# Optimization experiments

Measured on AMD Instinct MI355X. Metric: run time of the kernel, lower is better.

The kernel has to match this reference:

```python
import math
import jax, jax.numpy as jnp
import numpy as np

N_HEAD = 16
BLOCK_SIZE = 2048


def setup_inputs() -> dict:
    key = jax.random.key(0)
    ks = jax.random.split(key, 6)
    B, L, D = 2, 2048, 1024
    hs = D // N_HEAD
    s = 0.02
    return {
        "x": jax.random.normal(ks[0], (B, L, D), dtype=jnp.float32),
        "Wqkv": jax.random.normal(ks[1], (D, 3 * D), dtype=jnp.float32) * s,
        "bqkv": jax.random.normal(ks[2], (3 * D,), dtype=jnp.float32) * s,
        "Wproj": jax.random.normal(ks[3], (D, D), dtype=jnp.float32) * s,
        "bproj": jax.random.normal(ks[4], (D,), dtype=jnp.float32) * s,
        "Er": jax.random.normal(ks[5], (BLOCK_SIZE, hs), dtype=jnp.float32),
    }


def _skew(QEr):
    # QEr: [B, H, L, L] -> pad one zero column on the left, reshape, drop first row
    B, H, R, C = QEr.shape
    padded = jnp.pad(QEr, ((0, 0), (0, 0), (0, 0), (1, 0)))  # [B,H,R,C+1]
    reshaped = padded.reshape(B, H, C + 1, R)
    return reshaped[:, :, 1:, :]  # [B,H,R,C]


def reference(x, Wqkv, bqkv, Wproj, bproj, Er):
    B, L, D = x.shape
    H = N_HEAD
    hs = D // H
    qkv = x @ Wqkv + bqkv  # [B,L,3D]
    q, k, v = jnp.split(qkv, 3, axis=-1)
    q = q.reshape(B, L, H, hs).transpose(0, 2, 1, 3)  # [B,H,L,hs]
    k = k.reshape(B, L, H, hs).transpose(0, 2, 1, 3)
    v = v.reshape(B, L, H, hs).transpose(0, 2, 1, 3)

    Er_used = Er[BLOCK_SIZE - L:, :]           # [L, hs]
    QEr = jnp.einsum('bhld,md->bhlm', q, Er_used)  # q @ Er^T -> [B,H,L,L]
    Srel = _skew(QEr)

    scale = 1.0 / math.sqrt(hs)
    att = (jnp.einsum('bhld,bhmd->bhlm', q, k) + Srel) * scale
    causal = jnp.tril(jnp.ones((L, L), dtype=bool))
    att = jnp.where(causal[None, None], att, -jnp.inf)
    att = jax.nn.softmax(att, axis=-1)
    y = jnp.einsum('bhlm,bhmd->bhld', att, v)  # [B,H,L,hs]
    y = y.transpose(0, 2, 1, 3).reshape(B, L, D)
    return y @ Wproj + bproj
```

## Files before the change

### kernel.cpp

```cpp
#include <hip/hip_runtime.h>
#include <hip/hip_bf16.h>

#define LSEQ 2048
#define NH 16
#define HS 64
#define DIM 1024

typedef __attribute__((ext_vector_type(8))) short short8;
typedef __attribute__((ext_vector_type(4))) float f32x4;

typedef const __attribute__((address_space(1))) void g_void_t;
typedef __attribute__((address_space(3))) void s_void_t;

#define QSCALE 0.18033688011112042f

static __device__ __forceinline__ short f2bf(float f) {
  __hip_bfloat16 h = __float2bfloat16(f);
  return __builtin_bit_cast(short, h);
}

static __device__ __forceinline__ float fexp2(float x) {
#if __has_builtin(__builtin_amdgcn_exp2f)
  return __builtin_amdgcn_exp2f(x);
#else
  float r; asm("v_exp_f32 %0, %1" : "=v"(r) : "v"(x)); return r;
#endif
}

template<int CTRL>
static __device__ __forceinline__ float dpp_mov(float x) {
  return __builtin_bit_cast(float,
      __builtin_amdgcn_update_dpp(0, __builtin_bit_cast(int, x), CTRL, 0xF, 0xF, true));
}
static __device__ __forceinline__ float redmax16(float x) {
  x = fmaxf(x, dpp_mov<0xB1>(x));
  x = fmaxf(x, dpp_mov<0x4E>(x));
  x = fmaxf(x, dpp_mov<0x141>(x));
  x = fmaxf(x, dpp_mov<0x140>(x));
  return x;
}
static __device__ __forceinline__ float redsum16(float x) {
  x += dpp_mov<0xB1>(x);
  x += dpp_mov<0x4E>(x);
  x += dpp_mov<0x141>(x);
  x += dpp_mov<0x140>(x);
  return x;
}


__global__ void prep_kernel(const float* __restrict__ x, const float* __restrict__ Er,
                            const float* __restrict__ Wqkv, const float* __restrict__ Wproj,
                            short* __restrict__ xb, short* __restrict__ Erb,
                            short* __restrict__ WqkvT, short* __restrict__ WprojT) {
  __shared__ float tile[64][65];
  int bid = blockIdx.x;
  if (bid < 4224) {
    const float* in; short* out; int i0;
    if (bid < 4096) { in = x;  out = xb;  i0 = bid * 256; }
    else            { in = Er; out = Erb; i0 = (bid - 4096) * 256; }
    int i = i0 + threadIdx.x;
    float4 v = reinterpret_cast<const float4*>(in)[i];
    short4 o;
    o.x = f2bf(v.x); o.y = f2bf(v.y); o.z = f2bf(v.z); o.w = f2bf(v.w);
    reinterpret_cast<short4*>(out)[i] = o;
    return;
  }
  int id = bid - 4224;
  const float* W; short* Wt; int N, tx, ty;
  if (id < 768) { W = Wqkv;  Wt = WqkvT;  N = 3072; tx = id % 48; ty = id / 48; }
  else { id -= 768; W = Wproj; Wt = WprojT; N = 1024; tx = id % 16; ty = id / 16; }
  const int K = 1024;
  int k0 = ty * 64, n0 = tx * 64;
  int t = threadIdx.x;
  int r4 = t >> 6, cc = t & 63;
  for (int i = 0; i < 16; ++i) {
    int row = i * 4 + r4;
    tile[row][cc] = W[(size_t)(k0 + row) * N + (n0 + cc)];
  }
  __syncthreads();
  for (int i = 0; i < 16; ++i) {
    int row = i * 4 + r4;
    Wt[(size_t)(n0 + row) * K + (k0 + cc)] = f2bf(tile[cc][row]);
  }
}


template<int MODE>
__global__ __launch_bounds__(256, 2) void gemm_bt_kernel(
    const short* __restrict__ A, const short* __restrict__ Bt,
    const float* __restrict__ bias, int M, int N, int K,
    short* __restrict__ oq, short* __restrict__ ok, short* __restrict__ ov,
    float* __restrict__ of)
{
  __shared__ short Al[128 * 32];
  __shared__ short Bl[128 * 32];
  const int m0 = blockIdx.y * 128, n0 = blockIdx.x * 128;
  const int t = threadIdx.x;
  const int lane = t & 63, wave = t >> 6;
  const int wr = wave >> 1, wc = wave & 1;
  const int g = lane >> 4, c = lane & 15;
  f32x4 acc[4][4] = {};

  for (int k0 = 0; k0 < K; k0 += 32) {
    __syncthreads();
    for (int i = 0; i < 2; ++i) {
      int ch = i * 256 + t;
      int row = ch >> 2, c8 = ch & 3;
      __builtin_amdgcn_global_load_lds(
          (g_void_t*)(A + (size_t)(m0 + row) * K + k0 + c8 * 8),
          (s_void_t*)(Al + (i * 256 + wave * 64) * 8), 16, 0, 0);
      __builtin_amdgcn_global_load_lds(
          (g_void_t*)(Bt + (size_t)(n0 + row) * K + k0 + c8 * 8),
          (s_void_t*)(Bl + (i * 256 + wave * 64) * 8), 16, 0, 0);
    }
    __syncthreads();
    short8 af[4], bf[4];
#pragma unroll
    for (int mi = 0; mi < 4; ++mi) {
      int row = wr * 64 + mi * 16 + c;
      af[mi] = *reinterpret_cast<const short8*>(Al + row * 32 + g * 8);
    }
#pragma unroll
    for (int ni = 0; ni < 4; ++ni) {
      int row = wc * 64 + ni * 16 + c;
      bf[ni] = *reinterpret_cast<const short8*>(Bl + row * 32 + g * 8);
    }
#pragma unroll
    for (int mi = 0; mi < 4; ++mi)
#pragma unroll
      for (int ni = 0; ni < 4; ++ni)
        acc[mi][ni] = __builtin_amdgcn_mfma_f32_16x16x32_bf16(af[mi], bf[ni], acc[mi][ni], 0, 0, 0);
  }

#pragma unroll
  for (int mi = 0; mi < 4; ++mi)
#pragma unroll
    for (int ni = 0; ni < 4; ++ni) {
      int n = n0 + wc * 64 + ni * 16 + c;
      float bv = bias[n];
#pragma unroll
      for (int r = 0; r < 4; ++r) {
        int m = m0 + wr * 64 + mi * 16 + g * 4 + r;
        float val = acc[mi][ni][r] + bv;
        if (MODE == 0) {
          int which = n >> 10;
          int hh2 = (n >> 6) & 15;
          int d = n & 63;
          int b = m >> 11, ll = m & 2047;
          if (which == 0) {
            oq[(((size_t)b * NH + hh2) * LSEQ + ll) * HS + d] = f2bf(val * QSCALE);
          } else if (which == 1) {
            ok[(((size_t)b * NH + hh2) * LSEQ + ll) * HS + d] = f2bf(val);
          } else {
            ov[(((size_t)b * NH + hh2) * HS + d) * LSEQ + ll] = f2bf(val);
          }
        } else {
          of[(size_t)m * N + n] = val;
        }
      }
    }
}


__global__ __launch_bounds__(256, 2) void attn_kernel(
    const short* __restrict__ Qb, const short* __restrict__ Kb,
    const short* __restrict__ VTb, const short* __restrict__ Erb,
    short* __restrict__ Y)
{
  const int bid = blockIdx.x;
  const int pair = bid >> 5;
  const int bh = bid & 31;
  const int bb = bh >> 4, hh = bh & 15;
  const int t = threadIdx.x;
  const int lane = t & 63, wave = t >> 6;
  const int g = lane >> 4, c = lane & 15;
  const int r8 = lane >> 3;
  const int c16b = (lane & 7) * 16;

  __shared__ short Ql[64 * 64];
  __shared__ short Kl[2][64 * 64];
  __shared__ short Vl[2][64 * 64];
  __shared__ short El[4][64 * 64];
  __shared__ short Pl[4][16 * 64];

  auto process = [&](int qt) {
    const int l0 = qt * 64;
    const int base = 31 - qt;

    const short* Qg = Qb + ((size_t)bh * LSEQ + l0) * HS;
    for (int i = 0; i < 2; ++i) {
      int ch = i * 256 + t;
      int row = ch >> 3, c8 = ch & 7;
      uint4 v = *reinterpret_cast<const uint4*>(Qg + row * HS + c8 * 8);
      int byte = row * 128 + ((c8 * 16) ^ ((row & 7) << 4));
      *reinterpret_cast<uint4*>(reinterpret_cast<char*>(Ql) + byte) = v;
    }
    __syncthreads();

    short8 qf[2];
#pragma unroll
    for (int kk = 0; kk < 2; ++kk) {
      int row = wave * 16 + c;
      int byte = row * 128 + ((kk * 32 + g * 8) * 2 ^ ((row & 7) << 4));
      qf[kk] = *reinterpret_cast<const short8*>(reinterpret_cast<char*>(Ql) + byte);
    }

    f32x4 acc_o[4] = {};
    float mrun[4], lrun[4];
#pragma unroll
    for (int r = 0; r < 4; ++r) { mrun[r] = -1e30f; lrun[r] = 0.0f; }

    auto stage_KV = [&](int step, int sel) {
      const char* Kg = (const char*)(Kb + ((size_t)bh * LSEQ + step * 64) * HS);
#pragma unroll
      for (int j = 0; j < 2; ++j) {
        int row = wave * 16 + j * 8 + r8;
        __builtin_amdgcn_global_load_lds(
            (g_void_t*)(Kg + row * 128 + (c16b ^ ((row & 7) << 4))),
            (s_void_t*)(&Kl[sel][(wave * 16 + j * 8) * 64]), 16, 0, 0);
      }
#pragma unroll
      for (int j = 0; j < 2; ++j) {
        int row = wave * 16 + j * 8 + r8;
        const char* Vg = (const char*)(VTb + ((size_t)bh * HS + row) * LSEQ + step * 64);
        __builtin_amdgcn_global_load_lds(
            (g_void_t*)(Vg + (c16b ^ ((row & 7) << 4))),
            (s_void_t*)(&Vl[sel][(wave * 16 + j * 8) * 64]), 16, 0, 0);
      }
    };
    auto stage_E = [&](int chunk) {
      int slot = chunk & 3;
#pragma unroll
      for (int j = 0; j < 2; ++j) {
        int row = wave * 16 + j * 8 + r8;
        int e = chunk * 64 + row;
        if (e > LSEQ - 1) e = LSEQ - 1;
        __builtin_amdgcn_global_load_lds(
            (g_void_t*)((const char*)Erb + (size_t)e * 128 + (c16b ^ ((row & 7) << 4))),
            (s_void_t*)(&El[slot][(wave * 16 + j * 8) * 64]), 16, 0, 0);
      }
    };

    stage_KV(0, 0);
    stage_E(base);
    stage_E(base + 1);

    for (int s = 0; s <= qt; ++s) {
      const int sel = s & 1;
      const bool diag = (s == qt);

      if (s < qt) {
        stage_KV(s + 1, sel ^ 1);
        stage_E(base + s + 2);
        asm volatile("s_waitcnt vmcnt(6)" ::: "memory");
      } else {
        asm volatile("s_waitcnt vmcnt(0)" ::: "memory");
      }
      __builtin_amdgcn_s_barrier();
      __builtin_amdgcn_sched_barrier(0);

      __builtin_amdgcn_s_setprio(1);
      f32x4 ga[5];
#pragma unroll
      for (int s5 = 0; s5 < 5; ++s5) {
        int rb = ((3 - wave) + s5) * 16 + c;
        int phys = (((base + s + (rb >> 6)) & 3) << 6) | (rb & 63);
        ga[s5] = (f32x4){0.0f, 0.0f, 0.0f, 0.0f};
#pragma unroll
        for (int kk = 0; kk < 2; ++kk) {
          int byte = phys * 128 + (((kk * 32 + g * 8) * 2) ^ ((rb & 7) << 4));
          short8 ef = *reinterpret_cast<const short8*>((char*)El + byte);
          ga[s5] = __builtin_amdgcn_mfma_f32_16x16x32_bf16(qf[kk], ef, ga[s5], 0, 0, 0);
        }
      }

      f32x4 sa[4];
#pragma unroll
      for (int ns = 0; ns < 4; ++ns) {
        sa[ns] = (f32x4){0.0f, 0.0f, 0.0f, 0.0f};
#pragma unroll
        for (int kk = 0; kk < 2; ++kk) {
          int row = ns * 16 + c;
          int byte = row * 128 + (((kk * 32 + g * 8) * 2) ^ ((row & 7) << 4));
          short8 kf = *reinterpret_cast<const short8*>((char*)Kl[sel] + byte);
          sa[ns] = __builtin_amdgcn_mfma_f32_16x16x32_bf16(qf[kk], kf, sa[ns], 0, 0, 0);
        }
      }
      __builtin_amdgcn_s_setprio(0);

      float sv[4][4];
#pragma unroll
      for (int r = 0; r < 4; ++r) {
        int i4 = g * 4 + r;
        int u0 = c + 15 - i4;
        int srcl = (g << 4) | (u0 & 15);
        float bp[5];
#pragma unroll
        for (int s5 = 0; s5 < 5; ++s5) bp[s5] = __shfl(ga[s5][r], srcl, 64);
        bool lo = (u0 < 16);
#pragma unroll
        for (int ns = 0; ns < 4; ++ns) {
          float srel = lo ? bp[ns] : bp[ns + 1];
          float xx = sa[ns][r] + srel;
          if (diag && (ns * 16 + c > wave * 16 + i4)) xx = -1e30f;
          sv[ns][r] = xx;
        }
      }

      float mx[4];
      bool need = false;
#pragma unroll
      for (int r = 0; r < 4; ++r) {
        float m = fmaxf(fmaxf(sv[0][r], sv[1][r]), fmaxf(sv[2][r], sv[3][r]));
        mx[r] = redmax16(m);
        need = need || (mx[r] > mrun[r] + 4.0f);
      }
      if (__ballot(need)) {
#pragma unroll
        for (int r = 0; r < 4; ++r) {
          float mnew = fmaxf(mrun[r], mx[r]);
          float al = fexp2(mrun[r] - mnew);
          mrun[r] = mnew;
          lrun[r] *= al;
#pragma unroll
          for (int ns = 0; ns < 4; ++ns) acc_o[ns][r] *= al;
        }
      }
#pragma unroll
      for (int ns = 0; ns < 4; ++ns)
#pragma unroll
        for (int r = 0; r < 4; ++r)
          sv[ns][r] = fexp2(sv[ns][r] - mrun[r]);
#pragma unroll
      for (int r = 0; r < 4; ++r) {
        float s2 = (sv[0][r] + sv[1][r]) + (sv[2][r] + sv[3][r]);
        lrun[r] += redsum16(s2);
      }

      short* Pw = Pl[wave];
#pragma unroll
      for (int ns = 0; ns < 4; ++ns)
#pragma unroll
        for (int r = 0; r < 4; ++r) {
          int row = g * 4 + r;
          int byte = row * 128 + (((ns * 16 + c) * 2) ^ ((row & 7) << 4));
          *reinterpret_cast<short*>(reinterpret_cast<char*>(Pw) + byte) = f2bf(sv[ns][r]);
        }

      __builtin_amdgcn_s_setprio(1);
#pragma unroll
      for (int kk = 0; kk < 2; ++kk) {
        int kbyte = (kk * 32 + g * 8) * 2;
        int byteP = c * 128 + (kbyte ^ ((c & 7) << 4));
        short8 pf = *reinterpret_cast<const short8*>(reinterpret_cast<char*>(Pw) + byteP);
#pragma unroll
        for (int ns = 0; ns < 4; ++ns) {
          int rowV = ns * 16 + c;
          int byteV = rowV * 128 + (kbyte ^ ((rowV & 7) << 4));
          short8 vf = *reinterpret_cast<const short8*>((char*)Vl[sel] + byteV);
          acc_o[ns] = __builtin_amdgcn_mfma_f32_16x16x32_bf16(pf, vf, acc_o[ns], 0, 0, 0);
        }
      }
      __builtin_amdgcn_s_setprio(0);

      __builtin_amdgcn_sched_barrier(0);
      __builtin_amdgcn_s_barrier();
    }

#pragma unroll
    for (int ns = 0; ns < 4; ++ns)
#pragma unroll
      for (int r = 0; r < 4; ++r) {
        int row = g * 4 + r;
        int lg = l0 + wave * 16 + row;
        int d = ns * 16 + c;
        Y[((size_t)bb * LSEQ + lg) * DIM + hh * HS + d] = f2bf(acc_o[ns][r] / lrun[r]);
      }
  };

  process(31 - pair);
  process(pair);
}


extern "C" void kernel_launch(void* const* d_in, const int* in_sizes, int n_in,
                              void* d_out, int out_size, void* d_ws, size_t ws_size,
                              hipStream_t stream)
{
  const float* x     = (const float*)d_in[0];
  const float* Wqkv  = (const float*)d_in[1];
  const float* bqkv  = (const float*)d_in[2];
  const float* Wproj = (const float*)d_in[3];
  const float* bproj = (const float*)d_in[4];
  const float* Er    = (const float*)d_in[5];

  char* ws = (char*)d_ws;
  short* xb     = (short*)(ws + 0);
  short* WqkvT  = (short*)(ws + 8388608);
  short* WprojT = (short*)(ws + 14680064);
  short* Erb    = (short*)(ws + 16777216);
  short* qB     = (short*)(ws + 17039360);
  short* kB     = (short*)(ws + 25427968);
  short* vTB    = (short*)(ws + 33816576);
  short* yB     = (short*)(ws + 42205184);

  prep_kernel<<<dim3(5248), 256, 0, stream>>>(x, Er, Wqkv, Wproj, xb, Erb, WqkvT, WprojT);

  gemm_bt_kernel<0><<<dim3(3072 / 128, 4096 / 128), 256, 0, stream>>>(
      xb, WqkvT, bqkv, 4096, 3072, 1024, qB, kB, vTB, nullptr);

  attn_kernel<<<dim3(512), 256, 0, stream>>>(qB, kB, vTB, Erb, yB);

  gemm_bt_kernel<1><<<dim3(1024 / 128, 4096 / 128), 256, 0, stream>>>(
      yB, WprojT, bproj, 4096, 1024, 1024, nullptr, nullptr, nullptr, (float*)d_out);
}
```

Measured before the change: 147.7 us.

## Enlarge attention query tile to 128 rows with 8 waves sharing K/V/Er staging

```diff
diff --git a/kernel.cpp b/kernel.cpp
--- a/kernel.cpp
+++ b/kernel.cpp
@@ -162,7 +162,7 @@
 }
 
 
-__global__ __launch_bounds__(256, 2) void attn_kernel(
+__global__ __launch_bounds__(512, 1) void attn_kernel(
     const short* __restrict__ Qb, const short* __restrict__ Kb,
     const short* __restrict__ VTb, const short* __restrict__ Erb,
     short* __restrict__ Y)
@@ -177,191 +177,189 @@
   const int r8 = lane >> 3;
   const int c16b = (lane & 7) * 16;
 
-  __shared__ short Ql[64 * 64];
+  __shared__ short Ql[128 * 64];
   __shared__ short Kl[2][64 * 64];
   __shared__ short Vl[2][64 * 64];
   __shared__ short El[4][64 * 64];
-  __shared__ short Pl[4][16 * 64];
+  __shared__ short Pl[8][16 * 64];
 
   auto process = [&](int qt) {
-    const int l0 = qt * 64;
-    const int base = 31 - qt;
-
-    const short* Qg = Qb + ((size_t)bh * LSEQ + l0) * HS;
-    for (int i = 0; i < 2; ++i) {
-      int ch = i * 256 + t;
-      int row = ch >> 3, c8 = ch & 7;
-      uint4 v = *reinterpret_cast<const uint4*>(Qg + row * HS + c8 * 8);
-      int byte = row * 128 + ((c8 * 16) ^ ((row & 7) << 4));
-      *reinterpret_cast<uint4*>(reinterpret_cast<char*>(Ql) + byte) = v;
-    }
-    __syncthreads();
-
-    short8 qf[2];
-#pragma unroll
-    for (int kk = 0; kk < 2; ++kk) {
-      int row = wave * 16 + c;
-      int byte = row * 128 + ((kk * 32 + g * 8) * 2 ^ ((row & 7) << 4));
-      qf[kk] = *reinterpret_cast<const short8*>(reinterpret_cast<char*>(Ql) + byte);
-    }
-
-    f32x4 acc_o[4] = {};
-    float mrun[4], lrun[4];
-#pragma unroll
-    for (int r = 0; r < 4; ++r) { mrun[r] = -1e30f; lrun[r] = 0.0f; }
+    const int l0 = qt * 128;
+    const int base = 30 - 2 * qt;
+    const int nsteps = 2 * qt + 2;
 
     auto stage_KV = [&](int step, int sel) {
+      int row = wave * 8 + r8;
       const char* Kg = (const char*)(Kb + ((size_t)bh * LSEQ + step * 64) * HS);
-#pragma unroll
-      for (int j = 0; j < 2; ++j) {
-        int row = wave * 16 + j * 8 + r8;
-        __builtin_amdgcn_global_load_lds(
-            (g_void_t*)(Kg + row * 128 + (c16b ^ ((row & 7) << 4))),
-            (s_void_t*)(&Kl[sel][(wave * 16 + j * 8) * 64]), 16, 0, 0);
-      }
-#pragma unroll
-      for (int j = 0; j < 2; ++j) {
-        int row = wave * 16 + j * 8 + r8;
-        const char* Vg = (const char*)(VTb + ((size_t)bh * HS + row) * LSEQ + step * 64);
-        __builtin_amdgcn_global_load_lds(
-            (g_void_t*)(Vg + (c16b ^ ((row & 7) << 4))),
-            (s_void_t*)(&Vl[sel][(wave * 16 + j * 8) * 64]), 16, 0, 0);
-      }
+      __builtin_amdgcn_global_load_lds(
+          (g_void_t*)(Kg + row * 128 + (c16b ^ ((row & 7) << 4))),
+          (s_void_t*)(&Kl[sel][(wave * 8) * 64]), 16, 0, 0);
+      const char* Vg = (const char*)(VTb + ((size_t)bh * HS + row) * LSEQ + step * 64);
+      __builtin_amdgcn_global_load_lds(
+          (g_void_t*)(Vg + (c16b ^ ((row & 7) << 4))),
+          (s_void_t*)(&Vl[sel][(wave * 8) * 64]), 16, 0, 0);
     };
     auto stage_E = [&](int chunk) {
       int slot = chunk & 3;
-#pragma unroll
-      for (int j = 0; j < 2; ++j) {
-        int row = wave * 16 + j * 8 + r8;
-        int e = chunk * 64 + row;
-        if (e > LSEQ - 1) e = LSEQ - 1;
-        __builtin_amdgcn_global_load_lds(
-            (g_void_t*)((const char*)Erb + (size_t)e * 128 + (c16b ^ ((row & 7) << 4))),
-            (s_void_t*)(&El[slot][(wave * 16 + j * 8) * 64]), 16, 0, 0);
-      }
+      int row = wave * 8 + r8;
+      int e = chunk * 64 + row;
+      if (e > LSEQ - 1) e = LSEQ - 1;
+      __builtin_amdgcn_global_load_lds(
+          (g_void_t*)((const char*)Erb + (size_t)e * 128 + (c16b ^ ((row & 7) << 4))),
+          (s_void_t*)(&El[slot][(wave * 8) * 64]), 16, 0, 0);
     };
 
+    const char* Qg = (const char*)(Qb + ((size_t)bh * LSEQ + l0) * HS);
+#pragma unroll
+    for (int i = 0; i < 2; ++i) {
+      int row = i * 64 + wave * 8 + r8;
+      __builtin_amdgcn_global_load_lds(
+          (g_void_t*)(Qg + row * 128 + (c16b ^ ((row & 7) << 4))),
+          (s_void_t*)(&Ql[(i * 64 + wave * 8) * 64]), 16, 0, 0);
+    }
     stage_KV(0, 0);
-    stage_E(base);
-    stage_E(base + 1);
-
-    for (int s = 0; s <= qt; ++s) {
+    stage_E(base); stage_E(base + 1); stage_E(base + 2);
+
+    asm volatile("s_waitcnt vmcnt(5)" ::: "memory");
+    __builtin_amdgcn_s_barrier();
+    __builtin_amdgcn_sched_barrier(0);
+
+    short8 qf[2];
+#pragma unroll
+    for (int kk = 0; kk < 2; ++kk) {
+      int row = wave * 16 + c;
+      int byte = row * 128 + (((kk * 32 + g * 8) * 2) ^ ((row & 7) << 4));
+      qf[kk] = *reinterpret_cast<const short8*>((char*)Ql + byte);
+    }
+
+    f32x4 acc_o[4] = {};
+    float mrun[4], lrun[4];
+#pragma unroll
+    for (int r = 0; r < 4; ++r) { mrun[r] = -1e30f; lrun[r] = 0.0f; }
+
+    for (int s = 0; s < nsteps; ++s) {
       const int sel = s & 1;
-      const bool diag = (s == qt);
-
-      if (s < qt) {
+      const int cb = base + s;
+
+      if (s + 1 < nsteps) {
         stage_KV(s + 1, sel ^ 1);
-        stage_E(base + s + 2);
-        asm volatile("s_waitcnt vmcnt(6)" ::: "memory");
+        stage_E(cb + 3);
+        asm volatile("s_waitcnt vmcnt(3)" ::: "memory");
       } else {
         asm volatile("s_waitcnt vmcnt(0)" ::: "memory");
       }
       __builtin_amdgcn_s_barrier();
       __builtin_amdgcn_sched_barrier(0);
 
-      __builtin_amdgcn_s_setprio(1);
-      f32x4 ga[5];
-#pragma unroll
-      for (int s5 = 0; s5 < 5; ++s5) {
-        int rb = ((3 - wave) + s5) * 16 + c;
-        int phys = (((base + s + (rb >> 6)) & 3) << 6) | (rb & 63);
-        ga[s5] = (f32x4){0.0f, 0.0f, 0.0f, 0.0f};
+      const bool deadwave = (s == nsteps - 1) && (wave < 4);
+      if (!deadwave) {
+        const bool maskstep = (s >= 2 * qt);
+
+        __builtin_amdgcn_s_setprio(1);
+        f32x4 ga[5];
+#pragma unroll
+        for (int s5 = 0; s5 < 5; ++s5) {
+          int rb = ((7 - wave) + s5) * 16 + c;
+          int phys = (((cb + (rb >> 6)) & 3) << 6) | (rb & 63);
+          ga[s5] = (f32x4){0.0f, 0.0f, 0.0f, 0.0f};
+#pragma unroll
+          for (int kk = 0; kk < 2; ++kk) {
+            int byte = phys * 128 + (((kk * 32 + g * 8) * 2) ^ ((rb & 7) << 4));
+            short8 ef = *reinterpret_cast<const short8*>((char*)El + byte);
+            ga[s5] = __builtin_amdgcn_mfma_f32_16x16x32_bf16(qf[kk], ef, ga[s5], 0, 0, 0);
+          }
+        }
+
+        f32x4 sa[4];
+#pragma unroll
+        for (int ns = 0; ns < 4; ++ns) {
+          sa[ns] = (f32x4){0.0f, 0.0f, 0.0f, 0.0f};
+#pragma unroll
+          for (int kk = 0; kk < 2; ++kk) {
+            int row = ns * 16 + c;
+            int byte = row * 128 + (((kk * 32 + g * 8) * 2) ^ ((row & 7) << 4));
+            short8 kf = *reinterpret_cast<const short8*>((char*)Kl[sel] + byte);
+            sa[ns] = __builtin_amdgcn_mfma_f32_16x16x32_bf16(qf[kk], kf, sa[ns], 0, 0, 0);
+          }
+        }
+        __builtin_amdgcn_s_setprio(0);
+
+        float sv[4][4];
+#pragma unroll
+        for (int r = 0; r < 4; ++r) {
+          int i4 = g * 4 + r;
+          int u0 = c + 15 - i4;
+          int srcl = (g << 4) | (u0 & 15);
+          float bp[5];
+#pragma unroll
+          for (int s5 = 0; s5 < 5; ++s5) bp[s5] = __shfl(ga[s5][r], srcl, 64);
+          bool lo = (u0 < 16);
+          int thr = (l0 - 64 * s) + wave * 16 + i4;
+#pragma unroll
+          for (int ns = 0; ns < 4; ++ns) {
+            float srel = lo ? bp[ns] : bp[ns + 1];
+            float xx = sa[ns][r] + srel;
+            if (maskstep && (ns * 16 + c > thr)) xx = -1e30f;
+            sv[ns][r] = xx;
+          }
+        }
+
+        float mx[4];
+        bool need = false;
+#pragma unroll
+        for (int r = 0; r < 4; ++r) {
+          float m = fmaxf(fmaxf(sv[0][r], sv[1][r]), fmaxf(sv[2][r], sv[3][r]));
+          mx[r] = redmax16(m);
+          need = need || (mx[r] > mrun[r] + 4.0f);
+        }
+        if (__ballot(need)) {
+#pragma unroll
+          for (int r = 0; r < 4; ++r) {
+            float mnew = fmaxf(mrun[r], mx[r]);
+            float al = fexp2(mrun[r] - mnew);
+            mrun[r] = mnew;
+            lrun[r] *= al;
+#pragma unroll
+            for (int ns = 0; ns < 4; ++ns) acc_o[ns][r] *= al;
+          }
+        }
+#pragma unroll
+        for (int ns = 0; ns < 4; ++ns)
+#pragma unroll
+          for (int r = 0; r < 4; ++r)
+            sv[ns][r] = fexp2(sv[ns][r] - mrun[r]);
+#pragma unroll
+        for (int r = 0; r < 4; ++r) {
+          float s2 = (sv[0][r] + sv[1][r]) + (sv[2][r] + sv[3][r]);
+          lrun[r] += redsum16(s2);
+        }
+
+        short* Pw = Pl[wave];
+#pragma unroll
+        for (int ns = 0; ns < 4; ++ns)
+#pragma unroll
+          for (int r = 0; r < 4; ++r) {
+            int row = g * 4 + r;
+            int byte = row * 128 + (((ns * 16 + c) * 2) ^ ((row & 7) << 4));
+            *reinterpret_cast<short*>(reinterpret_cast<char*>(Pw) + byte) = f2bf(sv[ns][r]);
+          }
+
+        __builtin_amdgcn_s_setprio(1);
 #pragma unroll
         for (int kk = 0; kk < 2; ++kk) {
-          int byte = phys * 128 + (((kk * 32 + g * 8) * 2) ^ ((rb & 7) << 4));
-          short8 ef = *reinterpret_cast<const short8*>((char*)El + byte);
-          ga[s5] = __builtin_amdgcn_mfma_f32_16x16x32_bf16(qf[kk], ef, ga[s5], 0, 0, 0);
-        }
+          int kbyte = (kk * 32 + g * 8) * 2;
+          int byteP = c * 128 + (kbyte ^ ((c & 7) << 4));
+          short8 pf = *reinterpret_cast<const short8*>(reinterpret_cast<char*>(Pw) + byteP);
+#pragma unroll
+          for (int ns = 0; ns < 4; ++ns) {
+            int rowV = ns * 16 + c;
+            int byteV = rowV * 128 + (kbyte ^ ((rowV & 7) << 4));
+            short8 vf = *reinterpret_cast<const short8*>((char*)Vl[sel] + byteV);
+            acc_o[ns] = __builtin_amdgcn_mfma_f32_16x16x32_bf16(pf, vf, acc_o[ns], 0, 0, 0);
+          }
+        }
+        __builtin_amdgcn_s_setprio(0);
       }
-
-      f32x4 sa[4];
-#pragma unroll
-      for (int ns = 0; ns < 4; ++ns) {
-        sa[ns] = (f32x4){0.0f, 0.0f, 0.0f, 0.0f};
-#pragma unroll
-        for (int kk = 0; kk < 2; ++kk) {
-          int row = ns * 16 + c;
-          int byte = row * 128 + (((kk * 32 + g * 8) * 2) ^ ((row & 7) << 4));
-          short8 kf = *reinterpret_cast<const short8*>((char*)Kl[sel] + byte);
-          sa[ns] = __builtin_amdgcn_mfma_f32_16x16x32_bf16(qf[kk], kf, sa[ns], 0, 0, 0);
-        }
-      }
-      __builtin_amdgcn_s_setprio(0);
-
-      float sv[4][4];
-#pragma unroll
-      for (int r = 0; r < 4; ++r) {
-        int i4 = g * 4 + r;
-        int u0 = c + 15 - i4;
-        int srcl = (g << 4) | (u0 & 15);
-        float bp[5];
-#pragma unroll
-        for (int s5 = 0; s5 < 5; ++s5) bp[s5] = __shfl(ga[s5][r], srcl, 64);
-        bool lo = (u0 < 16);
-#pragma unroll
-        for (int ns = 0; ns < 4; ++ns) {
-          float srel = lo ? bp[ns] : bp[ns + 1];
-          float xx = sa[ns][r] + srel;
-          if (diag && (ns * 16 + c > wave * 16 + i4)) xx = -1e30f;
-          sv[ns][r] = xx;
-        }
-      }
-
-      float mx[4];
-      bool need = false;
-#pragma unroll
-      for (int r = 0; r < 4; ++r) {
-        float m = fmaxf(fmaxf(sv[0][r], sv[1][r]), fmaxf(sv[2][r], sv[3][r]));
-        mx[r] = redmax16(m);
-        need = need || (mx[r] > mrun[r] + 4.0f);
-      }
-      if (__ballot(need)) {
-#pragma unroll
-        for (int r = 0; r < 4; ++r) {
-          float mnew = fmaxf(mrun[r], mx[r]);
-          float al = fexp2(mrun[r] - mnew);
-          mrun[r] = mnew;
-          lrun[r] *= al;
-#pragma unroll
-          for (int ns = 0; ns < 4; ++ns) acc_o[ns][r] *= al;
-        }
-      }
-#pragma unroll
-      for (int ns = 0; ns < 4; ++ns)
-#pragma unroll
-        for (int r = 0; r < 4; ++r)
-          sv[ns][r] = fexp2(sv[ns][r] - mrun[r]);
-#pragma unroll
-      for (int r = 0; r < 4; ++r) {
-        float s2 = (sv[0][r] + sv[1][r]) + (sv[2][r] + sv[3][r]);
-        lrun[r] += redsum16(s2);
-      }
-
-      short* Pw = Pl[wave];
-#pragma unroll
-      for (int ns = 0; ns < 4; ++ns)
-#pragma unroll
-        for (int r = 0; r < 4; ++r) {
-          int row = g * 4 + r;
-          int byte = row * 128 + (((ns * 16 + c) * 2) ^ ((row & 7) << 4));
-          *reinterpret_cast<short*>(reinterpret_cast<char*>(Pw) + byte) = f2bf(sv[ns][r]);
-        }
-
-      __builtin_amdgcn_s_setprio(1);
-#pragma unroll
-      for (int kk = 0; kk < 2; ++kk) {
-        int kbyte = (kk * 32 + g * 8) * 2;
-        int byteP = c * 128 + (kbyte ^ ((c & 7) << 4));
-        short8 pf = *reinterpret_cast<const short8*>(reinterpret_cast<char*>(Pw) + byteP);
-#pragma unroll
-        for (int ns = 0; ns < 4; ++ns) {
-          int rowV = ns * 16 + c;
-          int byteV = rowV * 128 + (kbyte ^ ((rowV & 7) << 4));
-          short8 vf = *reinterpret_cast<const short8*>((char*)Vl[sel] + byteV);
-          acc_o[ns] = __builtin_amdgcn_mfma_f32_16x16x32_bf16(pf, vf, acc_o[ns], 0, 0, 0);
-        }
-      }
-      __builtin_amdgcn_s_setprio(0);
 
       __builtin_amdgcn_sched_barrier(0);
       __builtin_amdgcn_s_barrier();
@@ -378,7 +376,7 @@
       }
   };
 
-  process(31 - pair);
+  process(15 - pair);
   process(pair);
 }
 
@@ -409,7 +407,7 @@
   gemm_bt_kernel<0><<<dim3(3072 / 128, 4096 / 128), 256, 0, stream>>>(
       xb, WqkvT, bqkv, 4096, 3072, 1024, qB, kB, vTB, nullptr);
 
-  attn_kernel<<<dim3(512), 256, 0, stream>>>(qB, kB, vTB, Erb, yB);
+  attn_kernel<<<dim3(256), 512, 0, stream>>>(qB, kB, vTB, Erb, yB);
 
   gemm_bt_kernel<1><<<dim3(1024 / 128, 4096 / 128), 256, 0, stream>>>(
       yB, WprojT, bproj, 4096, 1024, 1024, nullptr, nullptr, nullptr, (float*)d_out);
```

Measured after the change: 156.0 us. +5.7%, slower.

## Use 128-row query tiles per block with two 16-row subtiles per wave

Applied to the files above, without the earlier changes.

```diff
diff --git a/kernel.cpp b/kernel.cpp
--- a/kernel.cpp
+++ b/kernel.cpp
@@ -168,218 +168,238 @@
     short* __restrict__ Y)
 {
   const int bid = blockIdx.x;
-  const int pair = bid >> 5;
+  const int qt = (bid < 256) ? (15 - (bid >> 5)) : ((bid - 256) >> 5);
   const int bh = bid & 31;
   const int bb = bh >> 4, hh = bh & 15;
   const int t = threadIdx.x;
-  const int lane = t & 63, wave = t >> 6;
+  const int lane = t & 63, w = t >> 6;
   const int g = lane >> 4, c = lane & 15;
   const int r8 = lane >> 3;
   const int c16b = (lane & 7) * 16;
 
-  __shared__ short Ql[64 * 64];
+  const int l0 = qt * 128;
+  const int c00 = 31 - 2 * qt;
+  const int nsteps = 2 * qt + 2;
+
   __shared__ short Kl[2][64 * 64];
   __shared__ short Vl[2][64 * 64];
   __shared__ short El[4][64 * 64];
-  __shared__ short Pl[4][16 * 64];
-
-  auto process = [&](int qt) {
-    const int l0 = qt * 64;
-    const int base = 31 - qt;
-
-    const short* Qg = Qb + ((size_t)bh * LSEQ + l0) * HS;
-    for (int i = 0; i < 2; ++i) {
-      int ch = i * 256 + t;
-      int row = ch >> 3, c8 = ch & 7;
-      uint4 v = *reinterpret_cast<const uint4*>(Qg + row * HS + c8 * 8);
-      int byte = row * 128 + ((c8 * 16) ^ ((row & 7) << 4));
-      *reinterpret_cast<uint4*>(reinterpret_cast<char*>(Ql) + byte) = v;
-    }
-    __syncthreads();
-
-    short8 qf[2];
-#pragma unroll
-    for (int kk = 0; kk < 2; ++kk) {
-      int row = wave * 16 + c;
-      int byte = row * 128 + ((kk * 32 + g * 8) * 2 ^ ((row & 7) << 4));
-      qf[kk] = *reinterpret_cast<const short8*>(reinterpret_cast<char*>(Ql) + byte);
-    }
-
-    f32x4 acc_o[4] = {};
-    float mrun[4], lrun[4];
-#pragma unroll
-    for (int r = 0; r < 4; ++r) { mrun[r] = -1e30f; lrun[r] = 0.0f; }
-
-    auto stage_KV = [&](int step, int sel) {
+  __shared__ short Pl[4][32 * 64];
+
+  short8 qf[2][2];
+#pragma unroll
+  for (int tt = 0; tt < 2; ++tt)
+#pragma unroll
+    for (int kk = 0; kk < 2; ++kk)
+      qf[tt][kk] = *reinterpret_cast<const short8*>(
+          Qb + ((size_t)bh * LSEQ + l0 + w * 32 + tt * 16 + c) * HS + kk * 32 + g * 8);
+
+  auto stage_KV = [&](int step, int sel) {
+    int row = w * 16 + (r8 & 7) + ((lane >> 6) * 8);
+#pragma unroll
+    for (int j = 0; j < 2; ++j) {
+      int rr = w * 16 + j * 8 + r8;
       const char* Kg = (const char*)(Kb + ((size_t)bh * LSEQ + step * 64) * HS);
-#pragma unroll
-      for (int j = 0; j < 2; ++j) {
-        int row = wave * 16 + j * 8 + r8;
-        __builtin_amdgcn_global_load_lds(
-            (g_void_t*)(Kg + row * 128 + (c16b ^ ((row & 7) << 4))),
-            (s_void_t*)(&Kl[sel][(wave * 16 + j * 8) * 64]), 16, 0, 0);
-      }
-#pragma unroll
-      for (int j = 0; j < 2; ++j) {
-        int row = wave * 16 + j * 8 + r8;
-        const char* Vg = (const char*)(VTb + ((size_t)bh * HS + row) * LSEQ + step * 64);
-        __builtin_amdgcn_global_load_lds(
-            (g_void_t*)(Vg + (c16b ^ ((row & 7) << 4))),
-            (s_void_t*)(&Vl[sel][(wave * 16 + j * 8) * 64]), 16, 0, 0);
-      }
-    };
-    auto stage_E = [&](int chunk) {
-      int slot = chunk & 3;
-#pragma unroll
-      for (int j = 0; j < 2; ++j) {
-        int row = wave * 16 + j * 8 + r8;
-        int e = chunk * 64 + row;
-        if (e > LSEQ - 1) e = LSEQ - 1;
-        __builtin_amdgcn_global_load_lds(
-            (g_void_t*)((const char*)Erb + (size_t)e * 128 + (c16b ^ ((row & 7) << 4))),
-            (s_void_t*)(&El[slot][(wave * 16 + j * 8) * 64]), 16, 0, 0);
-      }
-    };
-
-    stage_KV(0, 0);
-    stage_E(base);
-    stage_E(base + 1);
-
-    for (int s = 0; s <= qt; ++s) {
-      const int sel = s & 1;
-      const bool diag = (s == qt);
-
-      if (s < qt) {
-        stage_KV(s + 1, sel ^ 1);
-        stage_E(base + s + 2);
-        asm volatile("s_waitcnt vmcnt(6)" ::: "memory");
-      } else {
-        asm volatile("s_waitcnt vmcnt(0)" ::: "memory");
-      }
-      __builtin_amdgcn_s_barrier();
-      __builtin_amdgcn_sched_barrier(0);
+      __builtin_amdgcn_global_load_lds(
+          (g_void_t*)(Kg + rr * 128 + (c16b ^ ((rr & 7) << 4))),
+          (s_void_t*)(&Kl[sel][(w * 16 + j * 8) * 64]), 16, 0, 0);
+    }
+#pragma unroll
+    for (int j = 0; j < 2; ++j) {
+      int rr = w * 16 + j * 8 + r8;
+      const char* Vg = (const char*)(VTb + ((size_t)bh * HS + rr) * LSEQ + step * 64);
+      __builtin_amdgcn_global_load_lds(
+          (g_void_t*)(Vg + (c16b ^ ((rr & 7) << 4))),
+          (s_void_t*)(&Vl[sel][(w * 16 + j * 8) * 64]), 16, 0, 0);
+    }
+    (void)row;
+  };
+  auto stage_E = [&](int chunk) {
+    int slot = chunk & 3;
+#pragma unroll
+    for (int j = 0; j < 2; ++j) {
+      int rr = w * 16 + j * 8 + r8;
+      int e = chunk * 64 + rr;
+      if (e > LSEQ - 1) e = LSEQ - 1;
+      if (e < 0) e = 0;
+      __builtin_amdgcn_global_load_lds(
+          (g_void_t*)((const char*)Erb + (size_t)e * 128 + (c16b ^ ((rr & 7) << 4))),
+          (s_void_t*)(&El[slot][(w * 16 + j * 8) * 64]), 16, 0, 0);
+    }
+  };
+
+  stage_KV(0, 0);
+  stage_E(c00 - 1); stage_E(c00); stage_E(c00 + 1);
+
+  f32x4 acc_o[2][4] = {};
+  float mrun[2][4], lrun[2][4];
+#pragma unroll
+  for (int tt = 0; tt < 2; ++tt)
+#pragma unroll
+    for (int r = 0; r < 4; ++r) { mrun[tt][r] = -1e30f; lrun[tt][r] = 0.0f; }
+
+  for (int s = 0; s < nsteps; ++s) {
+    const int sel = s & 1;
+    const int c0 = c00 + s;
+
+    if (s + 1 < nsteps) {
+      stage_KV(s + 1, sel ^ 1);
+      stage_E(c0 + 2);
+      asm volatile("s_waitcnt vmcnt(6)" ::: "memory");
+    } else {
+      asm volatile("s_waitcnt vmcnt(0)" ::: "memory");
+    }
+    __builtin_amdgcn_s_barrier();
+    __builtin_amdgcn_sched_barrier(0);
+
+    const bool deadwave = (s == nsteps - 1) && (w < 2);
+    if (!deadwave) {
+      const bool maskstep = (s >= 2 * qt);
 
       __builtin_amdgcn_s_setprio(1);
-      f32x4 ga[5];
-#pragma unroll
-      for (int s5 = 0; s5 < 5; ++s5) {
-        int rb = ((3 - wave) + s5) * 16 + c;
-        int phys = (((base + s + (rb >> 6)) & 3) << 6) | (rb & 63);
-        ga[s5] = (f32x4){0.0f, 0.0f, 0.0f, 0.0f};
+      f32x4 ga[2][5];
+#pragma unroll
+      for (int tt = 0; tt < 2; ++tt)
+#pragma unroll
+        for (int s5 = 0; s5 < 5; ++s5) ga[tt][s5] = (f32x4){0.0f, 0.0f, 0.0f, 0.0f};
+#pragma unroll
+      for (int u = 0; u < 6; ++u) {
+        int rb = ((2 - 2 * w) + u) * 16 + c;
+        int chunk = c0 + (rb >> 6);
+        int phys = ((chunk & 3) << 6) | (rb & 63);
 #pragma unroll
         for (int kk = 0; kk < 2; ++kk) {
           int byte = phys * 128 + (((kk * 32 + g * 8) * 2) ^ ((rb & 7) << 4));
           short8 ef = *reinterpret_cast<const short8*>((char*)El + byte);
-          ga[s5] = __builtin_amdgcn_mfma_f32_16x16x32_bf16(qf[kk], ef, ga[s5], 0, 0, 0);
-        }
-      }
-
-      f32x4 sa[4];
+          if (u >= 1) ga[0][u - 1] = __builtin_amdgcn_mfma_f32_16x16x32_bf16(qf[0][kk], ef, ga[0][u - 1], 0, 0, 0);
+          if (u <= 4) ga[1][u]     = __builtin_amdgcn_mfma_f32_16x16x32_bf16(qf[1][kk], ef, ga[1][u], 0, 0, 0);
+        }
+      }
+
+      f32x4 sa[2][4];
+#pragma unroll
+      for (int tt = 0; tt < 2; ++tt)
+#pragma unroll
+        for (int ns = 0; ns < 4; ++ns) sa[tt][ns] = (f32x4){0.0f, 0.0f, 0.0f, 0.0f};
 #pragma unroll
       for (int ns = 0; ns < 4; ++ns) {
-        sa[ns] = (f32x4){0.0f, 0.0f, 0.0f, 0.0f};
 #pragma unroll
         for (int kk = 0; kk < 2; ++kk) {
           int row = ns * 16 + c;
           int byte = row * 128 + (((kk * 32 + g * 8) * 2) ^ ((row & 7) << 4));
           short8 kf = *reinterpret_cast<const short8*>((char*)Kl[sel] + byte);
-          sa[ns] = __builtin_amdgcn_mfma_f32_16x16x32_bf16(qf[kk], kf, sa[ns], 0, 0, 0);
+          sa[0][ns] = __builtin_amdgcn_mfma_f32_16x16x32_bf16(qf[0][kk], kf, sa[0][ns], 0, 0, 0);
+          sa[1][ns] = __builtin_amdgcn_mfma_f32_16x16x32_bf16(qf[1][kk], kf, sa[1][ns], 0, 0, 0);
         }
       }
       __builtin_amdgcn_s_setprio(0);
 
-      float sv[4][4];
-#pragma unroll
-      for (int r = 0; r < 4; ++r) {
-        int i4 = g * 4 + r;
-        int u0 = c + 15 - i4;
-        int srcl = (g << 4) | (u0 & 15);
-        float bp[5];
-#pragma unroll
-        for (int s5 = 0; s5 < 5; ++s5) bp[s5] = __shfl(ga[s5][r], srcl, 64);
-        bool lo = (u0 < 16);
-#pragma unroll
-        for (int ns = 0; ns < 4; ++ns) {
-          float srel = lo ? bp[ns] : bp[ns + 1];
-          float xx = sa[ns][r] + srel;
-          if (diag && (ns * 16 + c > wave * 16 + i4)) xx = -1e30f;
-          sv[ns][r] = xx;
-        }
-      }
-
-      float mx[4];
+      float sv[2][4][4];
       bool need = false;
-#pragma unroll
-      for (int r = 0; r < 4; ++r) {
-        float m = fmaxf(fmaxf(sv[0][r], sv[1][r]), fmaxf(sv[2][r], sv[3][r]));
-        mx[r] = redmax16(m);
-        need = need || (mx[r] > mrun[r] + 4.0f);
+      float mx[2][4];
+#pragma unroll
+      for (int tt = 0; tt < 2; ++tt) {
+#pragma unroll
+        for (int r = 0; r < 4; ++r) {
+          int i4 = g * 4 + r;
+          int u0 = c + 15 - i4;
+          int srcl = (g << 4) | (u0 & 15);
+          float bp[5];
+#pragma unroll
+          for (int s5 = 0; s5 < 5; ++s5) bp[s5] = __shfl(ga[tt][s5][r], srcl, 64);
+          bool lo = (u0 < 16);
+          int thr = (l0 - 64 * s) + w * 32 + tt * 16 + i4;
+#pragma unroll
+          for (int ns = 0; ns < 4; ++ns) {
+            float srel = lo ? bp[ns] : bp[ns + 1];
+            float xx = sa[tt][ns][r] + srel;
+            if (maskstep && (ns * 16 + c > thr)) xx = -1e30f;
+            sv[tt][ns][r] = xx;
+          }
+        }
+#pragma unroll
+        for (int r = 0; r < 4; ++r) {
+          float m = fmaxf(fmaxf(sv[tt][0][r], sv[tt][1][r]), fmaxf(sv[tt][2][r], sv[tt][3][r]));
+          mx[tt][r] = redmax16(m);
+          need = need || (mx[tt][r] > mrun[tt][r] + 4.0f);
+        }
       }
       if (__ballot(need)) {
 #pragma unroll
+        for (int tt = 0; tt < 2; ++tt)
+#pragma unroll
+          for (int r = 0; r < 4; ++r) {
+            float mnew = fmaxf(mrun[tt][r], mx[tt][r]);
+            float al = fexp2(mrun[tt][r] - mnew);
+            mrun[tt][r] = mnew;
+            lrun[tt][r] *= al;
+#pragma unroll
+            for (int ns = 0; ns < 4; ++ns) acc_o[tt][ns][r] *= al;
+          }
+      }
+#pragma unroll
+      for (int tt = 0; tt < 2; ++tt) {
+#pragma unroll
+        for (int ns = 0; ns < 4; ++ns)
+#pragma unroll
+          for (int r = 0; r < 4; ++r)
+            sv[tt][ns][r] = fexp2(sv[tt][ns][r] - mrun[tt][r]);
+#pragma unroll
         for (int r = 0; r < 4; ++r) {
-          float mnew = fmaxf(mrun[r], mx[r]);
-          float al = fexp2(mrun[r] - mnew);
-          mrun[r] = mnew;
-          lrun[r] *= al;
-#pragma unroll
-          for (int ns = 0; ns < 4; ++ns) acc_o[ns][r] *= al;
-        }
-      }
-#pragma unroll
-      for (int ns = 0; ns < 4; ++ns)
-#pragma unroll
-        for (int r = 0; r < 4; ++r)
-          sv[ns][r] = fexp2(sv[ns][r] - mrun[r]);
-#pragma unroll
-      for (int r = 0; r < 4; ++r) {
-        float s2 = (sv[0][r] + sv[1][r]) + (sv[2][r] + sv[3][r]);
-        lrun[r] += redsum16(s2);
-      }
-
-      short* Pw = Pl[wave];
-#pragma unroll
-      for (int ns = 0; ns < 4; ++ns)
-#pragma unroll
-        for (int r = 0; r < 4; ++r) {
-          int row = g * 4 + r;
-          int byte = row * 128 + (((ns * 16 + c) * 2) ^ ((row & 7) << 4));
-          *reinterpret_cast<short*>(reinterpret_cast<char*>(Pw) + byte) = f2bf(sv[ns][r]);
-        }
+          float s2 = (sv[tt][0][r] + sv[tt][1][r]) + (sv[tt][2][r] + sv[tt][3][r]);
+          lrun[tt][r] += redsum16(s2);
+        }
+      }
+
+      short* Pw = Pl[w];
+#pragma unroll
+      for (int tt = 0; tt < 2; ++tt)
+#pragma unroll
+        for (int ns = 0; ns < 4; ++ns)
+#pragma unroll
+          for (int r = 0; r < 4; ++r) {
+            int row = tt * 16 + g * 4 + r;
+            int byte = row * 128 + (((ns * 16 + c) * 2) ^ ((row & 7) << 4));
+            *reinterpret_cast<short*>(reinterpret_cast<char*>(Pw) + byte) = f2bf(sv[tt][ns][r]);
+          }
 
       __builtin_amdgcn_s_setprio(1);
 #pragma unroll
       for (int kk = 0; kk < 2; ++kk) {
         int kbyte = (kk * 32 + g * 8) * 2;
-        int byteP = c * 128 + (kbyte ^ ((c & 7) << 4));
-        short8 pf = *reinterpret_cast<const short8*>(reinterpret_cast<char*>(Pw) + byteP);
+        short8 pf[2];
+#pragma unroll
+        for (int tt = 0; tt < 2; ++tt) {
+          int rowP = tt * 16 + c;
+          int byteP = rowP * 128 + (kbyte ^ ((c & 7) << 4));
+          pf[tt] = *reinterpret_cast<const short8*>(reinterpret_cast<char*>(Pw) + byteP);
+        }
 #pragma unroll
         for (int ns = 0; ns < 4; ++ns) {
           int rowV = ns * 16 + c;
           int byteV = rowV * 128 + (kbyte ^ ((rowV & 7) << 4));
           short8 vf = *reinterpret_cast<const short8*>((char*)Vl[sel] + byteV);
-          acc_o[ns] = __builtin_amdgcn_mfma_f32_16x16x32_bf16(pf, vf, acc_o[ns], 0, 0, 0);
+          acc_o[0][ns] = __builtin_amdgcn_mfma_f32_16x16x32_bf16(pf[0], vf, acc_o[0][ns], 0, 0, 0);
+          acc_o[1][ns] = __builtin_amdgcn_mfma_f32_16x16x32_bf16(pf[1], vf, acc_o[1][ns], 0, 0, 0);
         }
       }
       __builtin_amdgcn_s_setprio(0);
-
-      __builtin_amdgcn_sched_barrier(0);
-      __builtin_amdgcn_s_barrier();
-    }
-
+    }
+
+    __builtin_amdgcn_sched_barrier(0);
+    __builtin_amdgcn_s_barrier();
+  }
+
+#pragma unroll
+  for (int tt = 0; tt < 2; ++tt)
 #pragma unroll
     for (int ns = 0; ns < 4; ++ns)
 #pragma unroll
       for (int r = 0; r < 4; ++r) {
-        int row = g * 4 + r;
-        int lg = l0 + wave * 16 + row;
+        int lg = l0 + w * 32 + tt * 16 + g * 4 + r;
         int d = ns * 16 + c;
-        Y[((size_t)bb * LSEQ + lg) * DIM + hh * HS + d] = f2bf(acc_o[ns][r] / lrun[r]);
-      }
-  };
-
-  process(31 - pair);
-  process(pair);
+        Y[((size_t)bb * LSEQ + lg) * DIM + hh * HS + d] = f2bf(acc_o[tt][ns][r] / lrun[tt][r]);
+      }
 }
 
 
```

Result: slower. 208.2 us (+41.0%).
